# Optimization experiments

Hardware: AMD Instinct MI355X
Metric: run time of the kernel (lower is better)

## Reference

```python
import jax, jax.numpy as jnp
import numpy as np

N_HEADS = 16

def _rope_tables(L, head_dim, dtype):
    inv_freq = 1.0 / (10000.0 ** (jnp.arange(0, head_dim, 2, dtype=jnp.float32) / head_dim))
    t = jnp.arange(L, dtype=jnp.float32)
    freqs = jnp.outer(t, inv_freq)            # [L, head_dim/2]
    emb = jnp.concatenate([freqs, freqs], -1)  # [L, head_dim]
    return jnp.cos(emb).astype(dtype), jnp.sin(emb).astype(dtype)

def _apply_rope(x, cos, sin):
    # x: [B, L, H, hd]; cos/sin: [1, L, 1, hd]
    half = x.shape[-1] // 2
    x1, x2 = x[..., :half], x[..., half:]
    x_rot = jnp.concatenate([-x2, x1], -1)
    return x * cos + x_rot * sin

def setup_inputs() -> dict:
    key = jax.random.key(0)
    ks = jax.random.split(key, 5)
    D = 1024
    s = 0.02
    return {
        "x": jax.random.normal(ks[0], (4, 2048, D), jnp.float32),
        "w_qkv": jax.random.normal(ks[1], (3 * D, D), jnp.float32) * s,
        "b_qkv": jax.random.normal(ks[2], (3 * D,), jnp.float32) * s,
        "w_out": jax.random.normal(ks[3], (D, D), jnp.float32) * s,
        "b_out": jax.random.normal(ks[4], (D,), jnp.float32) * s,
    }

def reference(x, w_qkv, b_qkv, w_out, b_out):
    B, L, D = x.shape
    H = N_HEADS
    hd = D // H
    scale = hd ** -0.5
    qkv = (x @ w_qkv.T + b_qkv).reshape(B, L, 3, H, hd)
    q, k, v = qkv[:, :, 0], qkv[:, :, 1], qkv[:, :, 2]  # [B,L,H,hd]
    cos, sin = _rope_tables(L, hd, x.dtype)
    cos = cos[None, :, None, :]
    sin = sin[None, :, None, :]
    q = _apply_rope(q, cos, sin)
    k = _apply_rope(k, cos, sin)
    # [B,H,L,L] scores, non-causal softmax
    attn = jnp.einsum('blhd,bmhd->bhlm', q, k) * scale
    attn = jax.nn.softmax(attn, axis=-1)
    out = jnp.einsum('bhlm,bmhd->blhd', attn, v).reshape(B, L, D)
    return out @ w_out.T + b_out
```

## Files before the change

kernel.cpp:

```cpp
#include <hip/hip_runtime.h>
#include <stdint.h>

typedef __attribute__((ext_vector_type(4))) float f32x4;
typedef __attribute__((ext_vector_type(8))) short bf16x8;
typedef __attribute__((ext_vector_type(4))) short s16x4;
typedef __attribute__((ext_vector_type(4))) float fp32x4;

#define QSCALE 0.18033688f

__device__ __forceinline__ short f2bf(float f) {
    union { float f; unsigned u; } v; v.f = f;
    unsigned u = v.u;
    unsigned r = u + 0x7fffu + ((u >> 16) & 1u);
    return (short)(r >> 16);
}
__device__ __forceinline__ unsigned cvtpk(float a, float b) {
    unsigned r;
    asm("v_cvt_pk_bf16_f32 %0, %1, %2" : "=v"(r) : "v"(a), "v"(b));
    return r;
}

__device__ __forceinline__ void gld_lds16(const void* g, void* l) {
    __builtin_amdgcn_global_load_lds(
        (const __attribute__((address_space(1))) unsigned int*)(uintptr_t)g,
        (__attribute__((address_space(3))) unsigned int*)(uintptr_t)l,
        16, 0, 0);
}

__global__ __launch_bounds__(256) void cast_kernel(const float* __restrict__ in,
                                                   short* __restrict__ out, int n) {
    int idx = (blockIdx.x * 256 + threadIdx.x) * 8;
    if (idx >= n) return;
    fp32x4 a = *(const fp32x4*)&in[idx];
    fp32x4 b = *(const fp32x4*)&in[idx + 4];
    union { unsigned w[4]; bf16x8 v; } u;
    u.w[0] = cvtpk(a[0], a[1]); u.w[1] = cvtpk(a[2], a[3]);
    u.w[2] = cvtpk(b[0], b[1]); u.w[3] = cvtpk(b[2], b[3]);
    *(bf16x8*)&out[idx] = u.v;
}

__global__ __launch_bounds__(256) void rope_table_kernel(float* __restrict__ tab) {
    int idx = blockIdx.x * 256 + threadIdx.x;
    int l = idx >> 5, d = idx & 31;
    float inv = expf(-(float)d / 32.f * logf(10000.f));
    float ang = (float)l * inv;
    tab[idx * 2 + 0] = cosf(ang);
    tab[idx * 2 + 1] = sinf(ang);
}

template<int MODE>
__global__ __launch_bounds__(512, 2) void gemm_bt(const short* __restrict__ A,
                                                  const short* __restrict__ B,
                                                  const float* __restrict__ bias,
                                                  void* __restrict__ Cout,
                                                  short* __restrict__ VTout,
                                                  const float* __restrict__ tab,
                                                  int M, int N, int K) {
    __shared__ short lds[3 * 24576];
    const int tid = threadIdx.x;
    const int lane = tid & 63, wave = tid >> 6;
    const int i15 = lane & 15, g = lane >> 4;
    const int wr = wave >> 1, wc = wave & 1;

    const int nbx = gridDim.x;
    const int nwg = nbx * gridDim.y;
    int bid = blockIdx.y * nbx + blockIdx.x;
    int sw = (bid & 7) * (nwg >> 3) + (bid >> 3);
    const int m0 = (sw / nbx) * 256;
    const int n0 = (sw % nbx) * 128;

    const int xr3 = i15 & 3, xb2 = (i15 >> 2) & 1;
    const int cLo = g ^ xr3;
    const int aoff0 = (wr * 64 + i15) * 64 + (xb2 * 4 + cLo) * 8;
    const int aoff1 = (wr * 64 + i15) * 64 + ((1 ^ xb2) * 4 + cLo) * 8;
    const int boff0 = (wc * 64 + i15) * 64 + (xb2 * 4 + cLo) * 8;
    const int boff1 = (wc * 64 + i15) * 64 + ((1 ^ xb2) * 4 + cLo) * 8;

    const int srow = tid >> 3;
    const int ss = (tid & 7) ^ (srow & 7);
    const short* a0 = A + (size_t)(m0 + srow) * K + ss * 8;
    const short* a1 = a0 + (size_t)64 * K;
    const short* a2 = a0 + (size_t)128 * K;
    const short* a3 = a0 + (size_t)192 * K;
    const short* b0 = B + (size_t)(n0 + srow) * K + ss * 8;
    const short* b1 = b0 + (size_t)64 * K;

#define ST_A(slot, r, p) do { gld_lds16(p, lds + (slot) * 24576 + ((r) * 512 + wave * 64) * 8); p += 64; } while (0)
#define ST_B(slot, r, p) do { gld_lds16(p, lds + (slot) * 24576 + 16384 + ((r) * 512 + wave * 64) * 8); p += 64; } while (0)

    ST_A(0, 0, a0); ST_A(0, 1, a1); ST_B(0, 0, b0);
    ST_A(0, 2, a2); ST_A(0, 3, a3); ST_B(0, 1, b1);
    ST_A(1, 0, a0); ST_A(1, 1, a1); ST_B(1, 0, b0);
    ST_A(1, 2, a2); ST_A(1, 3, a3); ST_B(1, 1, b1);

    f32x4 acc[4][4] = {};
    const int NT = K >> 6;
    int slc = 0;

    for (int t = 0; t < NT; ++t) {
        int sl2 = slc + 2; if (sl2 >= 3) sl2 -= 3;
        if (t == NT - 1) asm volatile("s_waitcnt vmcnt(0)" ::: "memory");
        else             asm volatile("s_waitcnt vmcnt(6)" ::: "memory");
        __builtin_amdgcn_s_barrier();
        __builtin_amdgcn_sched_barrier(0);

        const short* As_ = lds + slc * 24576;
        const short* Bs_ = As_ + 16384;
        const bool pre = (t + 2 < NT);

        if (pre) { ST_A(sl2, 0, a0); ST_A(sl2, 1, a1); ST_B(sl2, 0, b0); }
        bf16x8 af[4][2], bfr[2][2];
#pragma unroll
        for (int m = 0; m < 4; ++m) {
            af[m][0] = *(const bf16x8*)&As_[aoff0 + m * 1024];
            af[m][1] = *(const bf16x8*)&As_[aoff1 + m * 1024];
        }
#pragma unroll
        for (int n = 0; n < 2; ++n) {
            bfr[n][0] = *(const bf16x8*)&Bs_[boff0 + n * 1024];
            bfr[n][1] = *(const bf16x8*)&Bs_[boff1 + n * 1024];
        }
        __builtin_amdgcn_s_barrier();
        asm volatile("s_waitcnt lgkmcnt(0)" ::: "memory");
        __builtin_amdgcn_sched_barrier(0);
        __builtin_amdgcn_s_setprio(1);
#pragma unroll
        for (int m = 0; m < 4; ++m)
#pragma unroll
            for (int n = 0; n < 2; ++n)
#pragma unroll
                for (int ks = 0; ks < 2; ++ks)
                    acc[m][n] = __builtin_amdgcn_mfma_f32_16x16x32_bf16(af[m][ks], bfr[n][ks], acc[m][n], 0, 0, 0);
        __builtin_amdgcn_s_setprio(0);

        if (pre) { ST_A(sl2, 2, a2); ST_A(sl2, 3, a3); ST_B(sl2, 1, b1); }
        bf16x8 bfr2[2][2];
#pragma unroll
        for (int n = 0; n < 2; ++n) {
            bfr2[n][0] = *(const bf16x8*)&Bs_[boff0 + (n + 2) * 1024];
            bfr2[n][1] = *(const bf16x8*)&Bs_[boff1 + (n + 2) * 1024];
        }
        __builtin_amdgcn_s_barrier();
        asm volatile("s_waitcnt lgkmcnt(0)" ::: "memory");
        __builtin_amdgcn_sched_barrier(0);
        __builtin_amdgcn_s_setprio(1);
#pragma unroll
        for (int m = 0; m < 4; ++m)
#pragma unroll
            for (int n = 0; n < 2; ++n)
#pragma unroll
                for (int ks = 0; ks < 2; ++ks)
                    acc[m][n + 2] = __builtin_amdgcn_mfma_f32_16x16x32_bf16(af[m][ks], bfr2[n][ks], acc[m][n + 2], 0, 0, 0);
        __builtin_amdgcn_s_setprio(0);

        slc = (slc == 2) ? 0 : slc + 1;
    }
#undef ST_A
#undef ST_B

    if (MODE == 0) {
#pragma unroll
        for (int m = 0; m < 4; ++m)
#pragma unroll
            for (int n = 0; n < 4; ++n) {
                int col = n0 + wc * 64 + n * 16 + i15;
                float bcol = bias[col];
#pragma unroll
                for (int j = 0; j < 4; ++j) {
                    int row = m0 + wr * 64 + m * 16 + g * 4 + j;
                    ((float*)Cout)[(size_t)row * N + col] = acc[m][n][j] + bcol;
                }
            }
    } else {
        const int sec = n0 >> 10;
        if (sec < 2) {
            const float qs = (sec == 0) ? QSCALE : 1.0f;
            short* out = (short*)Cout;
#pragma unroll
            for (int m = 0; m < 4; ++m) {
#pragma unroll
                for (int pp = 0; pp < 2; ++pp) {
                    int d = pp * 16 + i15;
                    int collo = n0 + wc * 64 + pp * 16 + i15;
                    float blo = bias[collo], bhi = bias[collo + 32];
#pragma unroll
                    for (int j = 0; j < 4; ++j) {
                        int row = m0 + wr * 64 + m * 16 + g * 4 + j;
                        int l = row & 2047;
                        float2 cs = *(const float2*)&tab[(l * 32 + d) * 2];
                        float x1 = acc[m][pp][j] + blo;
                        float x2 = acc[m][pp + 2][j] + bhi;
                        out[(size_t)row * 3072 + collo]      = f2bf((x1 * cs.x - x2 * cs.y) * qs);
                        out[(size_t)row * 3072 + collo + 32] = f2bf((x2 * cs.x + x1 * cs.y) * qs);
                    }
                }
            }
        } else {
#pragma unroll
            for (int m = 0; m < 4; ++m) {
                int rbase = m0 + wr * 64 + m * 16 + g * 4;
                int lbase = rbase & 2047, bidx = rbase >> 11;
#pragma unroll
                for (int n = 0; n < 4; ++n) {
                    int vcol = (n0 - 2048) + wc * 64 + n * 16 + i15;
                    int h = vcol >> 6, d = vcol & 63;
                    float bb = bias[n0 + wc * 64 + n * 16 + i15];
                    union { unsigned w[2]; s16x4 v; } u;
                    u.w[0] = cvtpk(acc[m][n][0] + bb, acc[m][n][1] + bb);
                    u.w[1] = cvtpk(acc[m][n][2] + bb, acc[m][n][3] + bb);
                    *(s16x4*)&VTout[((size_t)(bidx * 16 + h) * 64 + d) * 2048 + lbase] = u.v;
                }
            }
        }
    }
}

__global__ __launch_bounds__(512, 8) void attn_kernel(const short* __restrict__ qkv,
                                                      const short* __restrict__ VT,
                                                      short* __restrict__ O) {
    __shared__ short Ks[2][64 * 64];
    __shared__ short Vs[2][64 * 64];
    int orig = blockIdx.x;
    int xcd = orig & 7, idx = orig >> 3;
    int bh = xcd * 8 + (idx >> 4), qt = idx & 15;
    int b = bh >> 4, h = bh & 15;
    int tid = threadIdx.x, lane = tid & 63, wave = tid >> 6;
    int i15 = lane & 15, g = lane >> 4;
    int q0 = qt * 128;

    size_t qrow = (size_t)(b * 2048 + q0 + wave * 16 + i15);
    bf16x8 qf[2];
    qf[0] = *(const bf16x8*)&qkv[qrow * 3072 + h * 64 + 0  + g * 8];
    qf[1] = *(const bf16x8*)&qkv[qrow * 3072 + h * 64 + 32 + g * 8];

    bf16x8 onesf;
#pragma unroll
    for (int e = 0; e < 8; ++e) onesf[e] = (short)0x3F80;

    const int srow = tid >> 3, ss8 = (tid & 7) ^ (srow & 7);
    const int sprow = (srow & 0x23) | ((srow & 0x10) >> 2) | ((srow & 0x0C) << 1);
    const short* kp = qkv + (size_t)(b * 2048) * 3072 + 1024 + h * 64
                      + (size_t)sprow * 3072 + ss8 * 8;
    const short* vp = VT + (size_t)bh * 64 * 2048 + (size_t)srow * 2048 + ss8 * 8;

    const int xr3 = i15 & 3, xb2 = (i15 >> 2) & 1;
    const int cLo = g ^ xr3;
    const int o0 = i15 * 64 + (xb2 * 4 + cLo) * 8;
    const int o1 = i15 * 64 + ((1 ^ xb2) * 4 + cLo) * 8;

    f32x4 acc_o[4] = {};
    f32x4 acc_l = {0.f, 0.f, 0.f, 0.f};

#define STAGE(bk, bv)                                        \
    do {                                                     \
        gld_lds16(kp, (bk) + wave * 512);                    \
        gld_lds16(vp, (bv) + wave * 512);                    \
        kp += 64 * 3072;                                     \
        vp += 64;                                            \
    } while (0)

    STAGE(Ks[0], Vs[0]);

    for (int t = 0; t < 32; ++t) {
        const int cur = t & 1;
        if (t > 0) {
            __builtin_amdgcn_s_barrier();
            __builtin_amdgcn_sched_barrier(0);
        }
        if (t + 1 < 32) {
            STAGE(Ks[cur ^ 1], Vs[cur ^ 1]);
            asm volatile("s_waitcnt vmcnt(2)" ::: "memory");
        } else {
            asm volatile("s_waitcnt vmcnt(0)" ::: "memory");
        }
        __builtin_amdgcn_s_barrier();
        __builtin_amdgcn_sched_barrier(0);

        const short* ks = Ks[cur];
        const short* vs = Vs[cur];

        f32x4 sa[4] = {};
        __builtin_amdgcn_s_setprio(1);
#pragma unroll
        for (int kb = 0; kb < 2; ++kb) {
            const int ko = kb ? o1 : o0;
#pragma unroll
            for (int jb = 0; jb < 4; ++jb) {
                bf16x8 kf = *(const bf16x8*)&ks[ko + jb * 1024];
                sa[jb] = __builtin_amdgcn_mfma_f32_16x16x32_bf16(kf, qf[kb], sa[jb], 0, 0, 0);
            }
        }
        __builtin_amdgcn_s_setprio(0);

        float p[4][4];
#pragma unroll
        for (int jb = 0; jb < 4; ++jb)
#pragma unroll
            for (int r = 0; r < 4; ++r)
                p[jb][r] = __builtin_amdgcn_exp2f(sa[jb][r]);

        bf16x8 pf[2];
#pragma unroll
        for (int kb = 0; kb < 2; ++kb) {
            union { unsigned w[4]; bf16x8 v; } u;
            u.w[0] = cvtpk(p[2 * kb][0],     p[2 * kb][1]);
            u.w[1] = cvtpk(p[2 * kb][2],     p[2 * kb][3]);
            u.w[2] = cvtpk(p[2 * kb + 1][0], p[2 * kb + 1][1]);
            u.w[3] = cvtpk(p[2 * kb + 1][2], p[2 * kb + 1][3]);
            pf[kb] = u.v;
        }

        __builtin_amdgcn_s_setprio(1);
#pragma unroll
        for (int db = 0; db < 4; ++db) {
#pragma unroll
            for (int kb = 0; kb < 2; ++kb) {
                bf16x8 vf = *(const bf16x8*)&vs[(kb ? o1 : o0) + db * 1024];
                acc_o[db] = __builtin_amdgcn_mfma_f32_16x16x32_bf16(pf[kb], vf, acc_o[db], 0, 0, 0);
            }
        }
        acc_l = __builtin_amdgcn_mfma_f32_16x16x32_bf16(pf[0], onesf, acc_l, 0, 0, 0);
        acc_l = __builtin_amdgcn_mfma_f32_16x16x32_bf16(pf[1], onesf, acc_l, 0, 0, 0);
        __builtin_amdgcn_s_setprio(0);
    }
#undef STAGE

    float linv4[4];
#pragma unroll
    for (int r = 0; r < 4; ++r) linv4[r] = 1.f / acc_l[r];
#pragma unroll
    for (int db = 0; db < 4; ++db) {
        int ocol = h * 64 + db * 16 + i15;
#pragma unroll
        for (int r = 0; r < 4; ++r) {
            int orow = b * 2048 + q0 + wave * 16 + g * 4 + r;
            O[(size_t)orow * 1024 + ocol] = f2bf(acc_o[db][r] * linv4[r]);
        }
    }
}

extern "C" void kernel_launch(void* const* d_in, const int* in_sizes, int n_in,
                              void* d_out, int out_size, void* d_ws, size_t ws_size,
                              hipStream_t stream) {
    const float* x     = (const float*)d_in[0];
    const float* w_qkv = (const float*)d_in[1];
    const float* b_qkv = (const float*)d_in[2];
    const float* w_out = (const float*)d_in[3];
    const float* b_out = (const float*)d_in[4];

    char* ws = (char*)d_ws;
    short* qkvb = (short*)(ws);
    short* xb   = (short*)(ws + 50331648);
    short* wqb  = (short*)(ws + 67108864);
    short* wob  = (short*)(ws + 73400320);
    short* VT   = (short*)(ws + 75497472);
    float* rt   = (float*)(ws + 92274688);
    short* Ob   = xb;

    cast_kernel<<<4096, 256, 0, stream>>>(x, xb, 8388608);
    cast_kernel<<<1536, 256, 0, stream>>>(w_qkv, wqb, 3145728);
    cast_kernel<<<512, 256, 0, stream>>>(w_out, wob, 1048576);
    rope_table_kernel<<<256, 256, 0, stream>>>(rt);

    gemm_bt<1><<<dim3(24, 32), 512, 0, stream>>>(xb, wqb, b_qkv, qkvb, VT, rt, 8192, 3072, 1024);
    attn_kernel<<<1024, 512, 0, stream>>>(qkvb, VT, Ob);
    gemm_bt<0><<<dim3(8, 32), 512, 0, stream>>>(Ob, wob, b_out, d_out, nullptr, nullptr, 8192, 1024, 1024);
}
```

Measured before the change: 175.7 us.

## Fuse prep kernels, add double-buffered QKV GEMM variant, widen attention KV tiles

Merges the three cast kernels and the RoPE table kernel into one launch, removing per-launch overhead. Adds an NSLOT template so the QKV GEMM uses two LDS slots and a 4-wave-group occupancy hint instead of three slots, trading prefetch depth for more resident workgroups. The attention kernel now stages 128 keys per iteration in two 64-key sub-tiles, halving the number of barriers and loop trips but doubling LDS use and lowering the occupancy hint from 8 to 4.

Result: faster. 170.4 us (-3.0%).

```diff
diff --git a/kernel.cpp b/kernel.cpp
--- a/kernel.cpp
+++ b/kernel.cpp
@@ -27,36 +27,46 @@
         16, 0, 0);
 }
 
-__global__ __launch_bounds__(256) void cast_kernel(const float* __restrict__ in,
-                                                   short* __restrict__ out, int n) {
-    int idx = (blockIdx.x * 256 + threadIdx.x) * 8;
-    if (idx >= n) return;
-    fp32x4 a = *(const fp32x4*)&in[idx];
-    fp32x4 b = *(const fp32x4*)&in[idx + 4];
-    union { unsigned w[4]; bf16x8 v; } u;
-    u.w[0] = cvtpk(a[0], a[1]); u.w[1] = cvtpk(a[2], a[3]);
-    u.w[2] = cvtpk(b[0], b[1]); u.w[3] = cvtpk(b[2], b[3]);
-    *(bf16x8*)&out[idx] = u.v;
-}
-
-__global__ __launch_bounds__(256) void rope_table_kernel(float* __restrict__ tab) {
-    int idx = blockIdx.x * 256 + threadIdx.x;
-    int l = idx >> 5, d = idx & 31;
-    float inv = expf(-(float)d / 32.f * logf(10000.f));
-    float ang = (float)l * inv;
-    tab[idx * 2 + 0] = cosf(ang);
-    tab[idx * 2 + 1] = sinf(ang);
-}
-
-template<int MODE>
-__global__ __launch_bounds__(512, 2) void gemm_bt(const short* __restrict__ A,
-                                                  const short* __restrict__ B,
-                                                  const float* __restrict__ bias,
-                                                  void* __restrict__ Cout,
-                                                  short* __restrict__ VTout,
-                                                  const float* __restrict__ tab,
-                                                  int M, int N, int K) {
-    __shared__ short lds[3 * 24576];
+__global__ __launch_bounds__(256) void prep_kernel(const float* __restrict__ x,
+                                                   const float* __restrict__ wq,
+                                                   const float* __restrict__ wo,
+                                                   short* __restrict__ xb,
+                                                   short* __restrict__ wqb,
+                                                   short* __restrict__ wob,
+                                                   float* __restrict__ tab) {
+    int bid = blockIdx.x, tid = threadIdx.x;
+    if (bid < 6144) {
+        const float* in; short* out; int base;
+        if (bid < 4096)      { in = x;  out = xb;  base = bid; }
+        else if (bid < 5632) { in = wq; out = wqb; base = bid - 4096; }
+        else                 { in = wo; out = wob; base = bid - 5632; }
+        int idx = (base * 256 + tid) * 8;
+        fp32x4 a = *(const fp32x4*)&in[idx];
+        fp32x4 b = *(const fp32x4*)&in[idx + 4];
+        union { unsigned w[4]; bf16x8 v; } u;
+        u.w[0] = cvtpk(a[0], a[1]); u.w[1] = cvtpk(a[2], a[3]);
+        u.w[2] = cvtpk(b[0], b[1]); u.w[3] = cvtpk(b[2], b[3]);
+        *(bf16x8*)&out[idx] = u.v;
+    } else {
+        int idx = (bid - 6144) * 256 + tid;
+        int l = idx >> 5, d = idx & 31;
+        float inv = expf(-(float)d / 32.f * logf(10000.f));
+        float ang = (float)l * inv;
+        tab[idx * 2 + 0] = cosf(ang);
+        tab[idx * 2 + 1] = sinf(ang);
+    }
+}
+
+template<int MODE, int NSLOT>
+__global__ __launch_bounds__(512, (NSLOT == 2 ? 4 : 2))
+void gemm_bt(const short* __restrict__ A,
+             const short* __restrict__ B,
+             const float* __restrict__ bias,
+             void* __restrict__ Cout,
+             short* __restrict__ VTout,
+             const float* __restrict__ tab,
+             int M, int N, int K) {
+    __shared__ short lds[NSLOT * 24576];
     const int tid = threadIdx.x;
     const int lane = tid & 63, wave = tid >> 6;
     const int i15 = lane & 15, g = lane >> 4;
@@ -88,27 +98,43 @@
 #define ST_A(slot, r, p) do { gld_lds16(p, lds + (slot) * 24576 + ((r) * 512 + wave * 64) * 8); p += 64; } while (0)
 #define ST_B(slot, r, p) do { gld_lds16(p, lds + (slot) * 24576 + 16384 + ((r) * 512 + wave * 64) * 8); p += 64; } while (0)
 
-    ST_A(0, 0, a0); ST_A(0, 1, a1); ST_B(0, 0, b0);
-    ST_A(0, 2, a2); ST_A(0, 3, a3); ST_B(0, 1, b1);
-    ST_A(1, 0, a0); ST_A(1, 1, a1); ST_B(1, 0, b0);
-    ST_A(1, 2, a2); ST_A(1, 3, a3); ST_B(1, 1, b1);
+    if (NSLOT == 3) {
+        ST_A(0, 0, a0); ST_A(0, 1, a1); ST_B(0, 0, b0);
+        ST_A(0, 2, a2); ST_A(0, 3, a3); ST_B(0, 1, b1);
+        ST_A(1, 0, a0); ST_A(1, 1, a1); ST_B(1, 0, b0);
+        ST_A(1, 2, a2); ST_A(1, 3, a3); ST_B(1, 1, b1);
+    } else {
+        ST_A(0, 0, a0); ST_A(0, 1, a1); ST_B(0, 0, b0);
+        ST_A(0, 2, a2); ST_A(0, 3, a3); ST_B(0, 1, b1);
+    }
 
     f32x4 acc[4][4] = {};
     const int NT = K >> 6;
     int slc = 0;
 
-    for (int t = 0; t < NT; ++t) {
-        int sl2 = slc + 2; if (sl2 >= 3) sl2 -= 3;
-        if (t == NT - 1) asm volatile("s_waitcnt vmcnt(0)" ::: "memory");
-        else             asm volatile("s_waitcnt vmcnt(6)" ::: "memory");
+    for (int T = 0; T < NT; ++T) {
+        int stslot;
+        if (NSLOT == 3) {
+            stslot = slc + 2; if (stslot >= 3) stslot -= 3;
+            if (T == NT - 1) asm volatile("s_waitcnt vmcnt(0)" ::: "memory");
+            else             asm volatile("s_waitcnt vmcnt(6)" ::: "memory");
+        } else {
+            stslot = slc ^ 1;
+            asm volatile("s_waitcnt vmcnt(0)" ::: "memory");
+        }
         __builtin_amdgcn_s_barrier();
         __builtin_amdgcn_sched_barrier(0);
 
         const short* As_ = lds + slc * 24576;
         const short* Bs_ = As_ + 16384;
-        const bool pre = (t + 2 < NT);
-
-        if (pre) { ST_A(sl2, 0, a0); ST_A(sl2, 1, a1); ST_B(sl2, 0, b0); }
+        const bool pre = (NSLOT == 3) ? (T + 2 < NT) : (T + 1 < NT);
+
+        if (NSLOT == 3) {
+            if (pre) { ST_A(stslot, 0, a0); ST_A(stslot, 1, a1); ST_B(stslot, 0, b0); }
+        } else {
+            if (pre) { ST_A(stslot, 0, a0); ST_A(stslot, 1, a1); ST_B(stslot, 0, b0);
+                       ST_A(stslot, 2, a2); ST_A(stslot, 3, a3); ST_B(stslot, 1, b1); }
+        }
         bf16x8 af[4][2], bfr[2][2];
 #pragma unroll
         for (int m = 0; m < 4; ++m) {
@@ -133,7 +159,7 @@
                     acc[m][n] = __builtin_amdgcn_mfma_f32_16x16x32_bf16(af[m][ks], bfr[n][ks], acc[m][n], 0, 0, 0);
         __builtin_amdgcn_s_setprio(0);
 
-        if (pre) { ST_A(sl2, 2, a2); ST_A(sl2, 3, a3); ST_B(sl2, 1, b1); }
+        if (NSLOT == 3 && pre) { ST_A(stslot, 2, a2); ST_A(stslot, 3, a3); ST_B(stslot, 1, b1); }
         bf16x8 bfr2[2][2];
 #pragma unroll
         for (int n = 0; n < 2; ++n) {
@@ -153,7 +179,8 @@
                     acc[m][n + 2] = __builtin_amdgcn_mfma_f32_16x16x32_bf16(af[m][ks], bfr2[n][ks], acc[m][n + 2], 0, 0, 0);
         __builtin_amdgcn_s_setprio(0);
 
-        slc = (slc == 2) ? 0 : slc + 1;
+        if (NSLOT == 3) { slc = (slc == 2) ? 0 : slc + 1; }
+        else            { slc ^= 1; }
     }
 #undef ST_A
 #undef ST_B
@@ -215,11 +242,11 @@
     }
 }
 
-__global__ __launch_bounds__(512, 8) void attn_kernel(const short* __restrict__ qkv,
+__global__ __launch_bounds__(512, 4) void attn_kernel(const short* __restrict__ qkv,
                                                       const short* __restrict__ VT,
                                                       short* __restrict__ O) {
-    __shared__ short Ks[2][64 * 64];
-    __shared__ short Vs[2][64 * 64];
+    __shared__ short Ks[2][2][64 * 64];
+    __shared__ short Vs[2][2][64 * 64];
     int orig = blockIdx.x;
     int xcd = orig & 7, idx = orig >> 3;
     int bh = xcd * 8 + (idx >> 4), qt = idx & 15;
@@ -251,77 +278,82 @@
     f32x4 acc_o[4] = {};
     f32x4 acc_l = {0.f, 0.f, 0.f, 0.f};
 
-#define STAGE(bk, bv)                                        \
-    do {                                                     \
-        gld_lds16(kp, (bk) + wave * 512);                    \
-        gld_lds16(vp, (bv) + wave * 512);                    \
-        kp += 64 * 3072;                                     \
-        vp += 64;                                            \
+#define STAGE(buf)                                            \
+    do {                                                      \
+        gld_lds16(kp,                  Ks[buf][0] + wave * 512); \
+        gld_lds16(kp + (size_t)64 * 3072, Ks[buf][1] + wave * 512); \
+        gld_lds16(vp,                  Vs[buf][0] + wave * 512); \
+        gld_lds16(vp + 64,             Vs[buf][1] + wave * 512); \
+        kp += (size_t)128 * 3072;                             \
+        vp += 128;                                            \
     } while (0)
 
-    STAGE(Ks[0], Vs[0]);
-
-    for (int t = 0; t < 32; ++t) {
+    STAGE(0);
+
+    for (int t = 0; t < 16; ++t) {
         const int cur = t & 1;
         if (t > 0) {
             __builtin_amdgcn_s_barrier();
             __builtin_amdgcn_sched_barrier(0);
         }
-        if (t + 1 < 32) {
-            STAGE(Ks[cur ^ 1], Vs[cur ^ 1]);
-            asm volatile("s_waitcnt vmcnt(2)" ::: "memory");
+        if (t + 1 < 16) {
+            STAGE(cur ^ 1);
+            asm volatile("s_waitcnt vmcnt(4)" ::: "memory");
         } else {
             asm volatile("s_waitcnt vmcnt(0)" ::: "memory");
         }
         __builtin_amdgcn_s_barrier();
         __builtin_amdgcn_sched_barrier(0);
 
-        const short* ks = Ks[cur];
-        const short* vs = Vs[cur];
-
-        f32x4 sa[4] = {};
-        __builtin_amdgcn_s_setprio(1);
-#pragma unroll
-        for (int kb = 0; kb < 2; ++kb) {
-            const int ko = kb ? o1 : o0;
-#pragma unroll
-            for (int jb = 0; jb < 4; ++jb) {
-                bf16x8 kf = *(const bf16x8*)&ks[ko + jb * 1024];
-                sa[jb] = __builtin_amdgcn_mfma_f32_16x16x32_bf16(kf, qf[kb], sa[jb], 0, 0, 0);
-            }
-        }
-        __builtin_amdgcn_s_setprio(0);
-
-        float p[4][4];
-#pragma unroll
-        for (int jb = 0; jb < 4; ++jb)
-#pragma unroll
-            for (int r = 0; r < 4; ++r)
-                p[jb][r] = __builtin_amdgcn_exp2f(sa[jb][r]);
-
-        bf16x8 pf[2];
-#pragma unroll
-        for (int kb = 0; kb < 2; ++kb) {
-            union { unsigned w[4]; bf16x8 v; } u;
-            u.w[0] = cvtpk(p[2 * kb][0],     p[2 * kb][1]);
-            u.w[1] = cvtpk(p[2 * kb][2],     p[2 * kb][3]);
-            u.w[2] = cvtpk(p[2 * kb + 1][0], p[2 * kb + 1][1]);
-            u.w[3] = cvtpk(p[2 * kb + 1][2], p[2 * kb + 1][3]);
-            pf[kb] = u.v;
-        }
-
-        __builtin_amdgcn_s_setprio(1);
-#pragma unroll
-        for (int db = 0; db < 4; ++db) {
+#pragma unroll
+        for (int sub = 0; sub < 2; ++sub) {
+            const short* ks = Ks[cur][sub];
+            const short* vs = Vs[cur][sub];
+
+            f32x4 sa[4] = {};
+            __builtin_amdgcn_s_setprio(1);
 #pragma unroll
             for (int kb = 0; kb < 2; ++kb) {
-                bf16x8 vf = *(const bf16x8*)&vs[(kb ? o1 : o0) + db * 1024];
-                acc_o[db] = __builtin_amdgcn_mfma_f32_16x16x32_bf16(pf[kb], vf, acc_o[db], 0, 0, 0);
-            }
-        }
-        acc_l = __builtin_amdgcn_mfma_f32_16x16x32_bf16(pf[0], onesf, acc_l, 0, 0, 0);
-        acc_l = __builtin_amdgcn_mfma_f32_16x16x32_bf16(pf[1], onesf, acc_l, 0, 0, 0);
-        __builtin_amdgcn_s_setprio(0);
+                const int ko = kb ? o1 : o0;
+#pragma unroll
+                for (int jb = 0; jb < 4; ++jb) {
+                    bf16x8 kf = *(const bf16x8*)&ks[ko + jb * 1024];
+                    sa[jb] = __builtin_amdgcn_mfma_f32_16x16x32_bf16(kf, qf[kb], sa[jb], 0, 0, 0);
+                }
+            }
+            __builtin_amdgcn_s_setprio(0);
+
+            float p[4][4];
+#pragma unroll
+            for (int jb = 0; jb < 4; ++jb)
+#pragma unroll
+                for (int r = 0; r < 4; ++r)
+                    p[jb][r] = __builtin_amdgcn_exp2f(sa[jb][r]);
+
+            bf16x8 pf[2];
+#pragma unroll
+            for (int kb = 0; kb < 2; ++kb) {
+                union { unsigned w[4]; bf16x8 v; } u;
+                u.w[0] = cvtpk(p[2 * kb][0],     p[2 * kb][1]);
+                u.w[1] = cvtpk(p[2 * kb][2],     p[2 * kb][3]);
+                u.w[2] = cvtpk(p[2 * kb + 1][0], p[2 * kb + 1][1]);
+                u.w[3] = cvtpk(p[2 * kb + 1][2], p[2 * kb + 1][3]);
+                pf[kb] = u.v;
+            }
+
+            __builtin_amdgcn_s_setprio(1);
+#pragma unroll
+            for (int db = 0; db < 4; ++db) {
+#pragma unroll
+                for (int kb = 0; kb < 2; ++kb) {
+                    bf16x8 vf = *(const bf16x8*)&vs[(kb ? o1 : o0) + db * 1024];
+                    acc_o[db] = __builtin_amdgcn_mfma_f32_16x16x32_bf16(pf[kb], vf, acc_o[db], 0, 0, 0);
+                }
+            }
+            acc_l = __builtin_amdgcn_mfma_f32_16x16x32_bf16(pf[0], onesf, acc_l, 0, 0, 0);
+            acc_l = __builtin_amdgcn_mfma_f32_16x16x32_bf16(pf[1], onesf, acc_l, 0, 0, 0);
+            __builtin_amdgcn_s_setprio(0);
+        }
     }
 #undef STAGE
 
@@ -357,12 +389,9 @@
     float* rt   = (float*)(ws + 92274688);
     short* Ob   = xb;
 
-    cast_kernel<<<4096, 256, 0, stream>>>(x, xb, 8388608);
-    cast_kernel<<<1536, 256, 0, stream>>>(w_qkv, wqb, 3145728);
-    cast_kernel<<<512, 256, 0, stream>>>(w_out, wob, 1048576);
-    rope_table_kernel<<<256, 256, 0, stream>>>(rt);
-
-    gemm_bt<1><<<dim3(24, 32), 512, 0, stream>>>(xb, wqb, b_qkv, qkvb, VT, rt, 8192, 3072, 1024);
+    prep_kernel<<<6400, 256, 0, stream>>>(x, w_qkv, w_out, xb, wqb, wob, rt);
+
+    gemm_bt<1, 2><<<dim3(24, 32), 512, 0, stream>>>(xb, wqb, b_qkv, qkvb, VT, rt, 8192, 3072, 1024);
     attn_kernel<<<1024, 512, 0, stream>>>(qkvb, VT, Ob);
-    gemm_bt<0><<<dim3(8, 32), 512, 0, stream>>>(Ob, wob, b_out, d_out, nullptr, nullptr, 8192, 1024, 1024);
-}
+    gemm_bt<0, 3><<<dim3(8, 32), 512, 0, stream>>>(Ob, wob, b_out, d_out, nullptr, nullptr, 8192, 1024, 1024);
+}
```
